# Optimization experiments

Measured on AMD Instinct MI355X. Metric: run time of the kernel, lower is better.

Reference implementation:

```python
import jax, jax.numpy as jnp
import numpy as np

EPS = 1e-8

def _fft_unit_proj(x):
    # Project each vector to unit magnitude in the Fourier domain (norm_kv=True).
    f = jnp.fft.fft(x, axis=-1)
    return jnp.real(jnp.fft.ifft(f / (jnp.abs(f) + EPS), axis=-1))

def _hrr_key_value_query(k, v, q, causal=True):
    # k, v, q: [B, S, D]
    k = _fft_unit_proj(k)
    v = _fft_unit_proj(v)
    # bind: circular convolution of key and value
    kv = jnp.real(jnp.fft.ifft(jnp.fft.fft(k, axis=-1) * jnp.fft.fft(v, axis=-1), axis=-1))
    # causal associative memory: running sum of bound pairs along sequence
    if causal:
        mem = jnp.cumsum(kv, axis=1)
    else:
        mem = jnp.broadcast_to(jnp.sum(kv, axis=1, keepdims=True), kv.shape)
    # unbind: circular correlation of memory with query
    out = jnp.real(jnp.fft.ifft(jnp.conj(jnp.fft.fft(q, axis=-1)) * jnp.fft.fft(mem, axis=-1), axis=-1))
    return out


def setup_inputs() -> dict:
    key = jax.random.key(0)
    ks = jax.random.split(key, 8)
    B, S, D = 2, 4096, 2048
    sc = 1.0 / np.sqrt(D).astype(np.float32)
    return {
        "hidden_states": jax.random.normal(ks[0], (B, S, D), jnp.float32),
        "base_output": jax.random.normal(ks[1], (B, S, D), jnp.float32),
        "Wq": jax.random.normal(ks[2], (D, D), jnp.float32) * sc,
        "bq": jnp.zeros((D,), jnp.float32),
        "Wk": jax.random.normal(ks[3], (D, D), jnp.float32) * sc,
        "bk": jnp.zeros((D,), jnp.float32),
        "Wv": jax.random.normal(ks[4], (D, D), jnp.float32) * sc,
        "bv": jnp.zeros((D,), jnp.float32),
        "gate": jax.random.normal(ks[5], (1,), jnp.float32) * 0.1,
    }


def reference(hidden_states, base_output, Wq, bq, Wk, bk, Wv, bv, gate):
    # Adapter q/k/v projections (nn.Linear uses y = x @ W.T + b)
    q = jnp.einsum('bsd,ed->bse', hidden_states, Wq) + bq
    k = jnp.einsum('bsd,ed->bse', hidden_states, Wk) + bk
    v = jnp.einsum('bsd,ed->bse', hidden_states, Wv) + bv
    adapter = _hrr_key_value_query(k, v, q, causal=True)
    return base_output + gate * adapter
```

## Files before the change

kernel.cpp:

```cpp
#include <hip/hip_runtime.h>
#include <math.h>

constexpr int D_DIM  = 2048;
constexpr int HALF_D = 1024;
constexpr int B_DIM  = 2;
constexpr int S_DIM  = 4096;
constexpr int NROW   = B_DIM * S_DIM;
constexpr int NCHUNK = 64;
constexpr int CHLEN  = S_DIM / NCHUNK;
constexpr float EPS_ = 1e-8f;

typedef __attribute__((ext_vector_type(8))) short  short8;
typedef __attribute__((ext_vector_type(8))) unsigned short ushort8;
typedef __attribute__((ext_vector_type(4))) float  f32x4;

__device__ __forceinline__ float2 mkf2(float x, float y){ float2 r; r.x=x; r.y=y; return r; }
__device__ __forceinline__ float2 cmulf(float2 a, float2 b){
  return mkf2(fmaf(a.x, b.x, -a.y*b.y), fmaf(a.x, b.y, a.y*b.x));
}
__device__ __forceinline__ unsigned short f2bf(float x){
  unsigned u = __float_as_uint(x);
  u += 0x7fff + ((u >> 16) & 1);
  return (unsigned short)(u >> 16);
}
__device__ __forceinline__ float bf2f(unsigned short h){
  return __uint_as_float(((unsigned)h) << 16);
}

__global__ __launch_bounds__(256)
void cvt_f32_bf16(const float* __restrict__ in, unsigned short* __restrict__ out, int n8)
{
  int i = blockIdx.x * 256 + threadIdx.x;
  if (i >= n8) return;
  const float4* p = (const float4*)in + (size_t)i * 2;
  float4 a = p[0], b = p[1];
  ushort8 o;
  o[0]=f2bf(a.x); o[1]=f2bf(a.y); o[2]=f2bf(a.z); o[3]=f2bf(a.w);
  o[4]=f2bf(b.x); o[5]=f2bf(b.y); o[6]=f2bf(b.z); o[7]=f2bf(b.w);
  *(ushort8*)(out + (size_t)i * 8) = o;
}

__global__ __launch_bounds__(512, 2)
void gemm_fused(const unsigned short* __restrict__ A,
                const unsigned short* __restrict__ Wc,
                const float* __restrict__ bq, const float* __restrict__ bk,
                const float* __restrict__ bv,
                unsigned short* __restrict__ qb, unsigned short* __restrict__ kvb)
{
  constexpr int K = 2048, NITER = 16;
  __shared__ unsigned short lds[65536];
  const int tid  = threadIdx.x;
  const int wid  = tid >> 6, lane = tid & 63;
  const int wr   = wid >> 2, wc = wid & 3;

  int bid = blockIdx.x;
  int sw  = (bid & 7) * 96 + (bid >> 3);
  const int bm = (sw / 24) * 256, bn = (sw % 24) * 256;

  const int srow = tid >> 3;
  const int skc  = ((tid & 7) ^ (srow & 7)) * 8;
  const unsigned short* Ag = A  + (size_t)(bm + srow) * K + skc;
  const unsigned short* Bg = Wc + (size_t)(bn + srow) * K + skc;
  unsigned short* Al = lds;
  unsigned short* Bl = lds + 32768;
  const int stoff = wid * 512;

  auto stA = [&](int kt, int d, int h, int r) {
    __builtin_amdgcn_global_load_lds(
      (const __attribute__((address_space(1))) void*)(Ag + (size_t)(h * 128 + r * 64) * K + kt * 64),
      (__attribute__((address_space(3))) void*)(Al + d * 16384 + h * 8192 + r * 4096 + stoff),
      16, 0, 0);
  };
  auto stB = [&](int kt, int d, int h, int r) {
    __builtin_amdgcn_global_load_lds(
      (const __attribute__((address_space(1))) void*)(Bg + (size_t)(h * 128 + r * 64) * K + kt * 64),
      (__attribute__((address_space(3))) void*)(Bl + d * 16384 + h * 8192 + r * 4096 + stoff),
      16, 0, 0);
  };

  const int frow = lane & 15;
  const int kq   = lane >> 4;
  int ksw[2];
  ksw[0] = ((0 * 4 + kq) ^ (frow & 7)) * 8;
  ksw[1] = ((1 * 4 + kq) ^ (frow & 7)) * 8;
  const int arow0 = (wr * 128 + frow) * 64;
  const int brow0 = (wc * 64 + frow) * 64;

  f32x4 acc[8][4];
#pragma unroll
  for (int i = 0; i < 8; ++i)
#pragma unroll
    for (int j = 0; j < 4; ++j) acc[i][j] = (f32x4){0.f, 0.f, 0.f, 0.f};

  stA(0, 0, 0, 0); stA(0, 0, 0, 1); stA(0, 0, 1, 0); stA(0, 0, 1, 1);
  stB(0, 0, 0, 0); stB(0, 0, 0, 1); stB(0, 0, 1, 0); stB(0, 0, 1, 1);
  stB(1, 1, 0, 0); stB(1, 1, 0, 1); stB(1, 1, 1, 0); stB(1, 1, 1, 1);
  asm volatile("s_waitcnt vmcnt(4)" ::: "memory");
  __builtin_amdgcn_s_barrier();
  __builtin_amdgcn_sched_barrier(0);

#pragma unroll 1
  for (int it = 0; it < NITER; ++it) {
    const bool nl = (it < NITER - 1);
    const int t1 = 2 * it + 1;
    short8 bfr[8];
#pragma unroll
    for (int ph = 0; ph < 8; ++ph) {
      const int g  = ph & 3;
      const int db = ph >> 2;
      const unsigned short* Ab = Al + db * 16384;
      const unsigned short* Bb = Bl + db * 16384;

      if      (ph == 0) { stA(t1, 1, 0, 0); stA(t1, 1, 0, 1); }
      else if (ph == 1) { stA(t1, 1, 1, 0); stA(t1, 1, 1, 1); }
      else if (ph == 2) { if (nl) { stB(t1 + 1, 0, 0, 0); stB(t1 + 1, 0, 0, 1); } }
      else if (ph == 3) { if (nl) { stB(t1 + 1, 0, 1, 0); stB(t1 + 1, 0, 1, 1); } }
      else if (ph == 4) { if (nl) { stA(t1 + 1, 0, 0, 0); stA(t1 + 1, 0, 0, 1); } }
      else if (ph == 5) { if (nl) { stA(t1 + 1, 0, 1, 0); stA(t1 + 1, 0, 1, 1); } }
      else if (ph == 6) { if (nl) { stB(t1 + 2, 1, 0, 0); stB(t1 + 2, 1, 0, 1); } }
      else              { if (nl) { stB(t1 + 2, 1, 1, 0); stB(t1 + 2, 1, 1, 1); } }

      short8 af[2][2];
#pragma unroll
      for (int q = 0; q < 2; ++q)
#pragma unroll
        for (int ks = 0; ks < 2; ++ks)
          af[q][ks] = *(const short8*)(Ab + arow0 + (2 * g + q) * 1024 + ksw[ks]);
      if (g == 0) {
#pragma unroll
        for (int nf = 0; nf < 4; ++nf)
#pragma unroll
          for (int ks = 0; ks < 2; ++ks)
            bfr[nf * 2 + ks] = *(const short8*)(Bb + brow0 + nf * 1024 + ksw[ks]);
      }

      __builtin_amdgcn_s_barrier();
      asm volatile("s_waitcnt lgkmcnt(0)" ::: "memory");
      __builtin_amdgcn_sched_barrier(0);
      __builtin_amdgcn_s_setprio(1);
#pragma unroll
      for (int ks = 0; ks < 2; ++ks)
#pragma unroll
        for (int q = 0; q < 2; ++q)
#pragma unroll
          for (int nf = 0; nf < 4; ++nf)
            acc[2 * g + q][nf] = __builtin_amdgcn_mfma_f32_16x16x32_bf16(
                af[q][ks], bfr[nf * 2 + ks], acc[2 * g + q][nf], 0, 0, 0);
      __builtin_amdgcn_s_setprio(0);

      if (ph == 3) {
        if (nl) asm volatile("s_waitcnt vmcnt(4)" ::: "memory");
        else    asm volatile("s_waitcnt vmcnt(0)" ::: "memory");
      } else if (ph == 7) {
        if (nl) asm volatile("s_waitcnt vmcnt(4)" ::: "memory");
      }
      __builtin_amdgcn_s_barrier();
    }
  }

  const int seg = bn >> 11;
  const float* bp = (seg == 0) ? bq : (seg == 1) ? bk : bv;
  float bias_j[4];
#pragma unroll
  for (int j = 0; j < 4; ++j)
    bias_j[j] = bp[(bn + wc * 64 + j * 16 + frow) & 2047];
  const int er = (lane >> 4) * 4;
  unsigned short* dst = (seg == 0) ? qb : kvb;
  const size_t rstride = (seg == 0) ? 2048 : 4096;
  const int coff = (seg == 2) ? 2048 : 0;
#pragma unroll
  for (int I = 0; I < 8; ++I) {
    int row = bm + wr * 128 + I * 16 + er;
#pragma unroll
    for (int j = 0; j < 4; ++j) {
      int col = (bn + wc * 64 + j * 16 + frow) & 2047;
#pragma unroll
      for (int r = 0; r < 4; ++r) {
        float val = acc[I][j][r] + bias_j[j];
        dst[(size_t)(row + r) * rstride + coff + col] = f2bf(val);
      }
    }
  }
}

__device__ __forceinline__ int XS(int i){ return i ^ (((i >> 5) ^ (i >> 10)) & 31); }
__device__ __forceinline__ int TS(int i){ return i ^ ((i >> 5) & 31); }

__device__ __forceinline__ float2 mulmi(float2 w){ return mkf2(w.y, -w.x); }
__device__ __forceinline__ float2 mulw8(float2 w){
  const float c = 0.70710678118654752f;
  return mkf2(c * (w.x + w.y), c * (w.y - w.x));
}
__device__ __forceinline__ void bfly(float2& a, float2& b, float2 w){
  float2 v = cmulf(w, b);
  b = mkf2(a.x - v.x, a.y - v.y);
  a = mkf2(a.x + v.x, a.y + v.y);
}
__device__ __forceinline__ void bflyc(float2& a, float2& b, float2 w){
  float2 d = mkf2(a.x - b.x, a.y - b.y);
  a = mkf2(a.x + b.x, a.y + b.y);
  b = mkf2(fmaf(d.x, w.x, d.y * w.y), fmaf(d.y, w.x, -d.x * w.y));
}

__device__ __forceinline__ void fwd8(float2 e[8], float2 wA, float2 wB0, float2 wC0){
  bfly(e[0], e[1], wA); bfly(e[2], e[3], wA); bfly(e[4], e[5], wA); bfly(e[6], e[7], wA);
  float2 wB1 = mulmi(wB0);
  bfly(e[0], e[2], wB0); bfly(e[1], e[3], wB1); bfly(e[4], e[6], wB0); bfly(e[5], e[7], wB1);
  float2 wC1 = mulw8(wC0), wC2 = mulmi(wC0), wC3 = mulmi(wC1);
  bfly(e[0], e[4], wC0); bfly(e[1], e[5], wC1); bfly(e[2], e[6], wC2); bfly(e[3], e[7], wC3);
}
__device__ __forceinline__ void inv8(float2 e[8], float2 wA, float2 wB0, float2 wC0){
  float2 wC1 = mulw8(wC0), wC2 = mulmi(wC0), wC3 = mulmi(wC1);
  bflyc(e[0], e[4], wC0); bflyc(e[1], e[5], wC1); bflyc(e[2], e[6], wC2); bflyc(e[3], e[7], wC3);
  float2 wB1 = mulmi(wB0);
  bflyc(e[0], e[2], wB0); bflyc(e[1], e[3], wB1); bflyc(e[4], e[6], wB0); bflyc(e[5], e[7], wB1);
  bflyc(e[0], e[1], wA); bflyc(e[2], e[3], wA); bflyc(e[4], e[5], wA); bflyc(e[6], e[7], wA);
}

__device__ __forceinline__ float2 twld(const float* twr, const float* twi, int i){
  int s = TS(i);
  return mkf2(twr[s], twi[s]);
}

__device__ void fft_fwd(float2* X, const float* twr, const float* twi, int t)
{
  const float2 one = mkf2(1.f, 0.f);
  {
    int b = 8 * t;
    float2 e[8];
#pragma unroll
    for (int r = 0; r < 8; ++r) e[r] = X[XS(b + r)];
    fwd8(e, one, one, one);
#pragma unroll
    for (int r = 0; r < 8; ++r) X[XS(b + r)] = e[r];
  }
  __syncthreads();
  {
    int u = t >> 5, b = 64 * (t & 31) + u;
    float2 e[8];
#pragma unroll
    for (int r = 0; r < 8; ++r) e[r] = X[XS(b + 8 * r)];
    fwd8(e, twld(twr,twi,128*u), twld(twr,twi,64*u), twld(twr,twi,32*u));
#pragma unroll
    for (int r = 0; r < 8; ++r) X[XS(b + 8 * r)] = e[r];
  }
  __syncthreads();
  {
    int u = t & 63, b = 512 * (t >> 6) + u;
    float2 e[8];
#pragma unroll
    for (int r = 0; r < 8; ++r) e[r] = X[XS(b + 64 * r)];
    fwd8(e, twld(twr,twi,16*u), twld(twr,twi,8*u), twld(twr,twi,4*u));
#pragma unroll
    for (int r = 0; r < 8; ++r) X[XS(b + 64 * r)] = e[r];
  }
  __syncthreads();
#pragma unroll
  for (int h = 0; h < 2; ++h) {
    int u = t + 256 * h;
    float2 f[4];
#pragma unroll
    for (int r = 0; r < 4; ++r) f[r] = X[XS(u + 512 * r)];
    float2 wA = twld(twr,twi,2*u), wB0 = twld(twr,twi,u), wB1 = mulmi(wB0);
    bfly(f[0], f[1], wA);  bfly(f[2], f[3], wA);
    bfly(f[0], f[2], wB0); bfly(f[1], f[3], wB1);
#pragma unroll
    for (int r = 0; r < 4; ++r) X[XS(u + 512 * r)] = f[r];
  }
  __syncthreads();
}

__device__ void fft_inv(float2* X, const float* twr, const float* twi, int t)
{
  const float2 one = mkf2(1.f, 0.f);
#pragma unroll
  for (int h = 0; h < 2; ++h) {
    int u = t + 256 * h;
    float2 f[4];
#pragma unroll
    for (int r = 0; r < 4; ++r) f[r] = X[XS(u + 512 * r)];
    float2 wA = twld(twr,twi,2*u), wB0 = twld(twr,twi,u), wB1 = mulmi(wB0);
    bflyc(f[0], f[2], wB0); bflyc(f[1], f[3], wB1);
    bflyc(f[0], f[1], wA);  bflyc(f[2], f[3], wA);
#pragma unroll
    for (int r = 0; r < 4; ++r) X[XS(u + 512 * r)] = f[r];
  }
  __syncthreads();
  {
    int u = t & 63, b = 512 * (t >> 6) + u;
    float2 e[8];
#pragma unroll
    for (int r = 0; r < 8; ++r) e[r] = X[XS(b + 64 * r)];
    inv8(e, twld(twr,twi,16*u), twld(twr,twi,8*u), twld(twr,twi,4*u));
#pragma unroll
    for (int r = 0; r < 8; ++r) X[XS(b + 64 * r)] = e[r];
  }
  __syncthreads();
  {
    int u = t >> 5, b = 64 * (t & 31) + u;
    float2 e[8];
#pragma unroll
    for (int r = 0; r < 8; ++r) e[r] = X[XS(b + 8 * r)];
    inv8(e, twld(twr,twi,128*u), twld(twr,twi,64*u), twld(twr,twi,32*u));
#pragma unroll
    for (int r = 0; r < 8; ++r) X[XS(b + 8 * r)] = e[r];
  }
  __syncthreads();
  {
    int b = 8 * t;
    float2 e[8];
#pragma unroll
    for (int r = 0; r < 8; ++r) e[r] = X[XS(b + r)];
    inv8(e, one, one, one);
#pragma unroll
    for (int r = 0; r < 8; ++r) X[XS(b + r)] = e[r];
  }
  __syncthreads();
}

__global__ __launch_bounds__(256)
void twiddle_init(float2* __restrict__ twg)
{
  int i = blockIdx.x * 256 + threadIdx.x;
  if (i < HALF_D) {
    float sv, cv;
    sincosf(-6.283185307179586f * (float)i / (float)D_DIM, &sv, &cv);
    twg[i] = mkf2(cv, sv);
  }
}

__global__ __launch_bounds__(256)
void fftkv_kernel(unsigned short* __restrict__ kvb, const float2* __restrict__ twg)
{
  __shared__ float2 X[D_DIM];
  __shared__ float twr[HALF_D], twi[HALF_D];
  const int t = threadIdx.x;
  const size_t row = blockIdx.x;
  const unsigned short* kvrow = kvb + row * 4096;

  for (int i = t; i < HALF_D; i += 256) {
    float2 w = twg[i]; int s = TS(i); twr[s] = w.x; twi[s] = w.y;
  }
  {
    int i0 = t * 8;
    ushort8 k8 = *(const ushort8*)(kvrow + i0);
    ushort8 v8 = *(const ushort8*)(kvrow + 2048 + i0);
#pragma unroll
    for (int r = 0; r < 8; ++r) {
      int i = i0 + r;
      int p = __brev((unsigned)i) >> 21;
      X[XS(p)] = mkf2(bf2f(k8[r]), bf2f(v8[r]));
    }
  }
  __syncthreads();
  fft_fwd(X, twr, twi, t);

  unsigned int* outp = (unsigned int*)(kvb + row * 4096);
  for (int d = t; d < HALF_D; d += 256) {
    float2 p;
    if (d == 0) {
      float2 z0 = X[XS(0)], zn = X[XS(HALF_D)];
      float k0 = z0.x, v0 = z0.y, kn = zn.x, vn = zn.y;
      float p0 = (k0 / (fabsf(k0) + EPS_)) * (v0 / (fabsf(v0) + EPS_));
      float pn = (kn / (fabsf(kn) + EPS_)) * (vn / (fabsf(vn) + EPS_));
      p = mkf2(p0, pn);
    } else {
      float2 A = X[XS(d)];
      float2 Bc = X[XS(D_DIM - d)];
      float2 Bj = mkf2(Bc.x, -Bc.y);
      float2 Fk = mkf2(0.5f * (A.x + Bj.x), 0.5f * (A.y + Bj.y));
      float2 tt = mkf2(0.5f * (A.x - Bj.x), 0.5f * (A.y - Bj.y));
      float2 Fv = mkf2(tt.y, -tt.x);
      float sa = 1.f / (sqrtf(Fk.x*Fk.x + Fk.y*Fk.y) + EPS_);
      float sb = 1.f / (sqrtf(Fv.x*Fv.x + Fv.y*Fv.y) + EPS_);
      p = cmulf(Fk, Fv);
      float sc = sa * sb;
      p.x *= sc; p.y *= sc;
    }
    outp[d] = (unsigned)f2bf(p.x) | ((unsigned)f2bf(p.y) << 16);
  }
}

__global__ __launch_bounds__(256)
void scan_partial(const unsigned short* __restrict__ kvb, float2* __restrict__ part)
{
  int gid = blockIdx.x * 256 + threadIdx.x;
  int q4 = gid & 255;
  int chunk = (gid >> 8) & (NCHUNK - 1);
  int b = gid >> 14;
  const unsigned short* p = kvb + (size_t)(b * S_DIM + chunk * CHLEN) * 4096 + q4 * 8;
  float ar[4] = {0,0,0,0}, ai[4] = {0,0,0,0};
  for (int s = 0; s < CHLEN; ++s) {
    ushort8 v = *(const ushort8*)(p + (size_t)s * 4096);
#pragma unroll
    for (int e = 0; e < 4; ++e) { ar[e] += bf2f(v[2*e]); ai[e] += bf2f(v[2*e+1]); }
  }
  float2* pp = part + (size_t)(b * NCHUNK + chunk) * HALF_D + q4 * 4;
#pragma unroll
  for (int e = 0; e < 4; ++e) pp[e] = mkf2(ar[e], ai[e]);
}

__global__ __launch_bounds__(256)
void scan_offsets(float2* __restrict__ part)
{
  int gid = blockIdx.x * 256 + threadIdx.x;
  int d = gid & (HALF_D - 1);
  int b = gid >> 10;
  float2* p = part + (size_t)b * (NCHUNK * HALF_D) + d;
  float2 acc = mkf2(0.f, 0.f);
  for (int c = 0; c < NCHUNK; ++c) {
    float2 v = p[(size_t)c * HALF_D];
    p[(size_t)c * HALF_D] = acc;
    acc.x += v.x; acc.y += v.y;
  }
}

__global__ __launch_bounds__(256)
void scan_apply(unsigned short* __restrict__ kvb, const float2* __restrict__ part)
{
  int gid = blockIdx.x * 256 + threadIdx.x;
  int q4 = gid & 255;
  int chunk = (gid >> 8) & (NCHUNK - 1);
  int b = gid >> 14;
  unsigned short* p = kvb + (size_t)(b * S_DIM + chunk * CHLEN) * 4096 + q4 * 8;
  const float2* pp = part + (size_t)(b * NCHUNK + chunk) * HALF_D + q4 * 4;
  float ar[4], ai[4];
#pragma unroll
  for (int e = 0; e < 4; ++e) { float2 v = pp[e]; ar[e] = v.x; ai[e] = v.y; }
  for (int s = 0; s < CHLEN; ++s) {
    ushort8 v = *(const ushort8*)(p + (size_t)s * 4096);
    ushort8 o;
#pragma unroll
    for (int e = 0; e < 4; ++e) {
      ar[e] += bf2f(v[2*e]); ai[e] += bf2f(v[2*e+1]);
      o[2*e] = f2bf(ar[e]); o[2*e+1] = f2bf(ai[e]);
    }
    *(ushort8*)(p + (size_t)s * 4096) = o;
  }
}

__global__ __launch_bounds__(256)
void final_kernel(const unsigned short* __restrict__ qb,
                  const unsigned short* __restrict__ kvb,
                  const float* __restrict__ base, const float* __restrict__ gate,
                  const float2* __restrict__ twg, float* __restrict__ out)
{
  __shared__ float2 X[D_DIM];
  __shared__ float twr[HALF_D], twi[HALF_D];
  const int t = threadIdx.x;
  const size_t row = blockIdx.x;
  const unsigned short* qrow = qb + row * 2048;
  const unsigned short* mrow = kvb + row * 4096;

  for (int i = t; i < HALF_D; i += 256) {
    float2 w = twg[i]; int s = TS(i); twr[s] = w.x; twi[s] = w.y;
  }
  {
    int i0 = t * 8;
    ushort8 q8 = *(const ushort8*)(qrow + i0);
#pragma unroll
    for (int r = 0; r < 8; ++r) {
      int i = i0 + r;
      int p = __brev((unsigned)i) >> 21;
      X[XS(p)] = mkf2(bf2f(q8[r]), 0.f);
    }
  }
  __syncthreads();
  fft_fwd(X, twr, twi, t);

  for (int d = t; d < HALF_D; d += 256) {
    float fmre = bf2f(mrow[2*d]), fmim = bf2f(mrow[2*d+1]);
    if (d == 0) {
      float2 f0 = X[XS(0)], f1 = X[XS(HALF_D)];
      X[XS(0)]      = mkf2(f0.x * fmre, -f0.y * fmre);
      X[XS(HALF_D)] = mkf2(f1.x * fmim, -f1.y * fmim);
    } else {
      float2 fq = X[XS(d)];
      X[XS(d)] = mkf2(fq.x*fmre + fq.y*fmim, fq.x*fmim - fq.y*fmre);
      float2 f2 = X[XS(D_DIM - d)];
      X[XS(D_DIM - d)] = mkf2(f2.x*fmre - f2.y*fmim, -f2.x*fmim - f2.y*fmre);
    }
  }
  __syncthreads();
  fft_inv(X, twr, twi, t);

  const float gv = gate[0] * (1.f / (float)D_DIM);
  const float* brow = base + row * D_DIM;
  float* orow = out + row * D_DIM;
  for (int i = t; i < D_DIM; i += 256) {
    int p = __brev((unsigned)i) >> 21;
    orow[i] = brow[i] + gv * X[XS(p)].x;
  }
}

extern "C" void kernel_launch(void* const* d_in, const int* in_sizes, int n_in,
                              void* d_out, int out_size, void* d_ws, size_t ws_size,
                              hipStream_t stream)
{
  const float* hs   = (const float*)d_in[0];
  const float* base = (const float*)d_in[1];
  const float* Wq   = (const float*)d_in[2];
  const float* bq   = (const float*)d_in[3];
  const float* Wk   = (const float*)d_in[4];
  const float* bk   = (const float*)d_in[5];
  const float* Wv   = (const float*)d_in[6];
  const float* bv   = (const float*)d_in[7];
  const float* gate = (const float*)d_in[8];
  float* out  = (float*)d_out;

  char* ws = (char*)d_ws;
  unsigned short* hsb = (unsigned short*)ws;
  unsigned short* wqb = (unsigned short*)(ws + 33554432);
  unsigned short* wkb = wqb + (size_t)D_DIM * D_DIM;
  unsigned short* wvb = wkb + (size_t)D_DIM * D_DIM;
  unsigned short* kvb = (unsigned short*)(ws + 58720256);
  unsigned short* qb  = (unsigned short*)(ws + 58720256 + 67108864);
  float2* part = (float2*)(ws + 58720256 + 67108864 + 33554432);
  float2* twg  = (float2*)ws;

  {
    int n8 = (NROW * D_DIM) / 8;
    cvt_f32_bf16<<<n8 / 256, 256, 0, stream>>>(hs, hsb, n8);
    int w8 = (D_DIM * D_DIM) / 8;
    cvt_f32_bf16<<<w8 / 256, 256, 0, stream>>>(Wq, wqb, w8);
    cvt_f32_bf16<<<w8 / 256, 256, 0, stream>>>(Wk, wkb, w8);
    cvt_f32_bf16<<<w8 / 256, 256, 0, stream>>>(Wv, wvb, w8);
  }

  gemm_fused<<<768, 512, 0, stream>>>(hsb, wqb, bq, bk, bv, qb, kvb);

  twiddle_init<<<4, 256, 0, stream>>>(twg);

  fftkv_kernel<<<NROW, 256, 0, stream>>>(kvb, twg);

  scan_partial<<<128, 256, 0, stream>>>(kvb, part);
  scan_offsets<<<(B_DIM * HALF_D) / 256, 256, 0, stream>>>(part);
  scan_apply<<<128, 256, 0, stream>>>(kvb, part);

  final_kernel<<<NROW, 256, 0, stream>>>(qb, kvb, base, gate, twg, out);
}
```

Before: 376.4 us.

## Pack two real rows per complex FFT in final kernel and fuse conversions

The final kernel now loads two query rows as the real and imaginary parts of one complex signal. It runs a single forward and inverse FFT for both, separates the two spectra using Hermitian symmetry before multiplying by each row's memory spectrum, and writes two output rows per block. This halves the FFT work and the block count in the last stage. Separately, the four f32-to-bf16 conversion launches are merged into one kernel to cut launch overhead, at the cost of a little more per-thread index arithmetic.

```diff
diff --git a/kernel.cpp b/kernel.cpp
--- a/kernel.cpp
+++ b/kernel.cpp
@@ -28,16 +28,30 @@
 }
 
 __global__ __launch_bounds__(256)
-void cvt_f32_bf16(const float* __restrict__ in, unsigned short* __restrict__ out, int n8)
-{
+void cvt_inputs(const float* __restrict__ hs, const float* __restrict__ Wq,
+                const float* __restrict__ Wk, const float* __restrict__ Wv,
+                unsigned short* __restrict__ hsb, unsigned short* __restrict__ wb)
+{
+  constexpr int n8 = (NROW * D_DIM) / 8;
+  constexpr int w8 = (D_DIM * D_DIM) / 8;
   int i = blockIdx.x * 256 + threadIdx.x;
-  if (i >= n8) return;
-  const float4* p = (const float4*)in + (size_t)i * 2;
+  const float* src;
+  unsigned short* dst;
+  int local;
+  if (i < n8) { src = hs; local = i; dst = hsb + (size_t)i * 8; }
+  else {
+    int j = i - n8;
+    int seg = j >> 19;
+    local = j & (w8 - 1);
+    src = (seg == 0) ? Wq : (seg == 1) ? Wk : Wv;
+    dst = wb + (size_t)j * 8;
+  }
+  const float4* p = (const float4*)src + (size_t)local * 2;
   float4 a = p[0], b = p[1];
   ushort8 o;
   o[0]=f2bf(a.x); o[1]=f2bf(a.y); o[2]=f2bf(a.z); o[3]=f2bf(a.w);
   o[4]=f2bf(b.x); o[5]=f2bf(b.y); o[6]=f2bf(b.z); o[7]=f2bf(b.w);
-  *(ushort8*)(out + (size_t)i * 8) = o;
+  *(ushort8*)dst = o;
 }
 
 __global__ __launch_bounds__(512, 2)
@@ -448,48 +462,60 @@
   __shared__ float2 X[D_DIM];
   __shared__ float twr[HALF_D], twi[HALF_D];
   const int t = threadIdx.x;
-  const size_t row = blockIdx.x;
-  const unsigned short* qrow = qb + row * 2048;
-  const unsigned short* mrow = kvb + row * 4096;
+  const size_t row0 = (size_t)blockIdx.x * 2;
+  const unsigned short* qrow = qb + row0 * 2048;
+  const unsigned short* m0 = kvb + row0 * 4096;
+  const unsigned short* m1 = m0 + 4096;
 
   for (int i = t; i < HALF_D; i += 256) {
     float2 w = twg[i]; int s = TS(i); twr[s] = w.x; twi[s] = w.y;
   }
   {
     int i0 = t * 8;
-    ushort8 q8 = *(const ushort8*)(qrow + i0);
+    ushort8 q0 = *(const ushort8*)(qrow + i0);
+    ushort8 q1 = *(const ushort8*)(qrow + 2048 + i0);
 #pragma unroll
     for (int r = 0; r < 8; ++r) {
       int i = i0 + r;
       int p = __brev((unsigned)i) >> 21;
-      X[XS(p)] = mkf2(bf2f(q8[r]), 0.f);
+      X[XS(p)] = mkf2(bf2f(q0[r]), bf2f(q1[r]));
     }
   }
   __syncthreads();
   fft_fwd(X, twr, twi, t);
 
   for (int d = t; d < HALF_D; d += 256) {
-    float fmre = bf2f(mrow[2*d]), fmim = bf2f(mrow[2*d+1]);
     if (d == 0) {
-      float2 f0 = X[XS(0)], f1 = X[XS(HALF_D)];
-      X[XS(0)]      = mkf2(f0.x * fmre, -f0.y * fmre);
-      X[XS(HALF_D)] = mkf2(f1.x * fmim, -f1.y * fmim);
+      float2 z0 = X[XS(0)], zn = X[XS(HALF_D)];
+      float M00 = bf2f(m0[0]), M0N = bf2f(m0[1]);
+      float M10 = bf2f(m1[0]), M1N = bf2f(m1[1]);
+      X[XS(0)]      = mkf2(z0.x * M00, z0.y * M10);
+      X[XS(HALF_D)] = mkf2(zn.x * M0N, zn.y * M1N);
     } else {
-      float2 fq = X[XS(d)];
-      X[XS(d)] = mkf2(fq.x*fmre + fq.y*fmim, fq.x*fmim - fq.y*fmre);
-      float2 f2 = X[XS(D_DIM - d)];
-      X[XS(D_DIM - d)] = mkf2(f2.x*fmre - f2.y*fmim, -f2.x*fmim - f2.y*fmre);
+      float2 Zd = X[XS(d)];
+      float2 Zn = X[XS(D_DIM - d)];
+      float2 Fq0 = mkf2(0.5f * (Zd.x + Zn.x), 0.5f * (Zd.y - Zn.y));
+      float2 td  = mkf2(0.5f * (Zd.x - Zn.x), 0.5f * (Zd.y + Zn.y));
+      float2 Fq1 = mkf2(td.y, -td.x);
+      float2 M0d = mkf2(bf2f(m0[2*d]), bf2f(m0[2*d+1]));
+      float2 M1d = mkf2(bf2f(m1[2*d]), bf2f(m1[2*d+1]));
+      float2 G0 = mkf2(Fq0.x*M0d.x + Fq0.y*M0d.y, Fq0.x*M0d.y - Fq0.y*M0d.x);
+      float2 G1 = mkf2(Fq1.x*M1d.x + Fq1.y*M1d.y, Fq1.x*M1d.y - Fq1.y*M1d.x);
+      X[XS(d)]         = mkf2(G0.x - G1.y, G0.y + G1.x);
+      X[XS(D_DIM - d)] = mkf2(G0.x + G1.y, G1.x - G0.y);
     }
   }
   __syncthreads();
   fft_inv(X, twr, twi, t);
 
   const float gv = gate[0] * (1.f / (float)D_DIM);
-  const float* brow = base + row * D_DIM;
-  float* orow = out + row * D_DIM;
+  const float* brow = base + row0 * 2048;
+  float* orow = out + row0 * 2048;
   for (int i = t; i < D_DIM; i += 256) {
     int p = __brev((unsigned)i) >> 21;
-    orow[i] = brow[i] + gv * X[XS(p)].x;
+    float2 y = X[XS(p)];
+    orow[i]        = brow[i]        + gv * y.x;
+    orow[2048 + i] = brow[2048 + i] + gv * y.y;
   }
 }
 
@@ -511,20 +537,15 @@
   char* ws = (char*)d_ws;
   unsigned short* hsb = (unsigned short*)ws;
   unsigned short* wqb = (unsigned short*)(ws + 33554432);
-  unsigned short* wkb = wqb + (size_t)D_DIM * D_DIM;
-  unsigned short* wvb = wkb + (size_t)D_DIM * D_DIM;
   unsigned short* kvb = (unsigned short*)(ws + 58720256);
   unsigned short* qb  = (unsigned short*)(ws + 58720256 + 67108864);
   float2* part = (float2*)(ws + 58720256 + 67108864 + 33554432);
   float2* twg  = (float2*)ws;
 
   {
-    int n8 = (NROW * D_DIM) / 8;
-    cvt_f32_bf16<<<n8 / 256, 256, 0, stream>>>(hs, hsb, n8);
-    int w8 = (D_DIM * D_DIM) / 8;
-    cvt_f32_bf16<<<w8 / 256, 256, 0, stream>>>(Wq, wqb, w8);
-    cvt_f32_bf16<<<w8 / 256, 256, 0, stream>>>(Wk, wkb, w8);
-    cvt_f32_bf16<<<w8 / 256, 256, 0, stream>>>(Wv, wvb, w8);
+    constexpr int n8 = (NROW * D_DIM) / 8;
+    constexpr int w8 = (D_DIM * D_DIM) / 8;
+    cvt_inputs<<<(n8 + 3 * w8) / 256, 256, 0, stream>>>(hs, Wq, Wk, Wv, hsb, wqb);
   }
 
   gemm_fused<<<768, 512, 0, stream>>>(hsb, wqb, bq, bk, bv, qb, kvb);
@@ -537,5 +558,5 @@
   scan_offsets<<<(B_DIM * HALF_D) / 256, 256, 0, stream>>>(part);
   scan_apply<<<128, 256, 0, stream>>>(kvb, part);
 
-  final_kernel<<<NROW, 256, 0, stream>>>(qb, kvb, base, gate, twg, out);
-}
+  final_kernel<<<NROW / 2, 256, 0, stream>>>(qb, kvb, base, gate, twg, out);
+}
```

Result: faster. 351.3 us (median of 2 runs) (-6.7%).
